# Kernel tuning notes

Measured on AMD Instinct MI355X. Metric: run time of the kernel, lower is better.

Reference implementation:

```python
import jax, jax.numpy as jnp
import numpy as np

L = 2          # lags
D = 16         # latent_size (number of per-channel MLPs)
H = 64         # hidden_dim
SLOPE = 0.2    # LeakyReLU negative slope used by NLayerLeakyMLP


def _forward(x, W0, b0, W1, b1, W2, b2, Wout, bout):
    B, T, _ = x.shape
    nwin = T - L
    # sliding windows of size L+1 along time: [B, nwin, L+1, D]
    idx = jnp.arange(nwin)[:, None] + jnp.arange(L + 1)[None, :]
    w = x[:, idx]
    N = B * nwin
    yy = w[:, :, :L, :].reshape(N, L * D)   # past L steps, flattened
    xx = w[:, :, L, :].reshape(N, D)        # current step, per channel
    # per-channel MLP inputs, stacked over channels: [D, N, L*D+1]
    inputs = jnp.concatenate(
        [jnp.broadcast_to(yy[None], (D, N, L * D)), xx.T[:, :, None]], axis=-1)

    def mlp(inp):  # all D channel-MLPs at once
        h = jax.nn.leaky_relu(jnp.einsum('dni,dhi->dnh', inp, W0) + b0[:, None, :], SLOPE)
        h = jax.nn.leaky_relu(jnp.einsum('dnh,dkh->dnk', h, W1) + b1[:, None, :], SLOPE)
        h = jax.nn.leaky_relu(jnp.einsum('dnh,dkh->dnk', h, W2) + b2[:, None, :], SLOPE)
        return jnp.einsum('dnh,doh->dno', h, Wout) + bout[:, None, :]  # [D, N, 1]

    # d g_i(inputs)/d (last coord) via one forward-mode JVP (replaces the
    # full batched Jacobian + diagonal extraction of the torch version)
    tangent = jnp.zeros_like(inputs).at[..., -1].set(1.0)
    out, dout = jax.jvp(mlp, (inputs,), (tangent,))
    residuals = out[:, :, 0].T.reshape(B, nwin, D)
    logabsdet = jnp.log(jnp.abs(dout[:, :, 0])).sum(0)          # sum over channels -> [N]
    sum_log_abs_det = logabsdet.reshape(B, nwin).sum(1)          # [B]
    return residuals, sum_log_abs_det


def setup_inputs():
    key = jax.random.key(0)
    ks = jax.random.split(key, 9)
    B, T = 32, 512
    in_f = L * D + 1
    s = 0.1
    return {
        "x": jax.random.normal(ks[0], (B, T, D), jnp.float32),
        "W0": jax.random.normal(ks[1], (D, H, in_f), jnp.float32) * s,
        "b0": jax.random.normal(ks[2], (D, H), jnp.float32) * s,
        "W1": jax.random.normal(ks[3], (D, H, H), jnp.float32) * s,
        "b1": jax.random.normal(ks[4], (D, H), jnp.float32) * s,
        "W2": jax.random.normal(ks[5], (D, H, H), jnp.float32) * s,
        "b2": jax.random.normal(ks[6], (D, H), jnp.float32) * s,
        "Wout": jax.random.normal(ks[7], (D, 1, H), jnp.float32) * s,
        "bout": jax.random.normal(ks[8], (D, 1), jnp.float32) * s,
    }


def reference(x, W0, b0, W1, b1, W2, b2, Wout, bout):
    return _forward(x, W0, b0, W1, b1, W2, b2, Wout, bout)
```

## Files before the change

kernel.cpp:

```cpp
#include <hip/hip_runtime.h>
#include <hip/hip_bf16.h>
#include <math.h>

#define NB 32
#define SEQT 512
#define DDIM 16
#define NWIN 510
#define NTOT (NB*NWIN)
#define SLOPE 0.2f
#define NI 3
#define GW 192
#define NGR 85
#define NGP 88

typedef __attribute__((ext_vector_type(8))) short sh8;
typedef __attribute__((ext_vector_type(4))) float f4;

#define W0B_OFF 0
#define W1B_OFF 65536
#define W2B_OFF 196608
#define WCOL_OFF 327680
#define RED_OFF 331776
#define NPREP 164864

static __device__ __forceinline__ unsigned short bfb(float f){
    union { __hip_bfloat16 h; unsigned short u; } cv;
    cv.h = __float2bfloat16(f);
    return cv.u;
}
static __device__ __forceinline__ unsigned pk2(float a, float b){
    return (unsigned)bfb(a) | ((unsigned)bfb(b) << 16);
}

__global__ void prep(const float* __restrict__ W0, const float* __restrict__ W1,
                     const float* __restrict__ W2, unsigned char* __restrict__ wsb){
    int e = blockIdx.x*256 + threadIdx.x;
    if (e < 32768){
        unsigned short* W0b = (unsigned short*)(wsb + W0B_OFF);
        int d = e >> 11, r = e & 2047, h = r >> 5, k = r & 31;
        W0b[e] = bfb(W0[(d*64 + h)*33 + k]);
    } else if (e < 98304){
        ((unsigned short*)(wsb + W1B_OFF))[e - 32768] = bfb(W1[e - 32768]);
    } else if (e < 163840){
        ((unsigned short*)(wsb + W2B_OFF))[e - 98304] = bfb(W2[e - 98304]);
    } else if (e < NPREP){
        int i = e - 163840;
        int d = i >> 6, h = i & 63;
        ((float*)(wsb + WCOL_OFF))[i] = W0[(d*64 + h)*33 + 32];
    }
}

__global__ __launch_bounds__(256, 3) void mlp(
    const float* __restrict__ x,
    const float* __restrict__ bias0, const float* __restrict__ bias1,
    const float* __restrict__ bias2,
    const float* __restrict__ Wout, const float* __restrict__ boutp,
    const unsigned char* __restrict__ wsb,
    float* __restrict__ red, float* __restrict__ out)
{
    __shared__ __align__(16) unsigned char bufA[GW*128];
    __shared__ __align__(16) unsigned char bufB[GW*128];

    const int tid  = threadIdx.x;
    const int lane = tid & 63;
    const int w    = tid >> 6;
    const int nl   = lane & 15;
    const int hi   = lane >> 4;
    const int rsw  = (nl & 7) << 4;

    const int bid = blockIdx.x;
    const int d   = (bid >> 3) & 15;
    const int g   = ((bid >> 7) << 3) | (bid & 7);
    if (g >= NGR) return;

    const unsigned char* W0b = wsb + W0B_OFF + d*4096;
    const unsigned char* W1b = wsb + W1B_OFF + d*8192;
    const unsigned char* W2b = wsb + W2B_OFF + d*8192;

    int   bb[NI], ttv[NI];
    float xxv[NI];
    union { uint4 u; sh8 s; } in[NI];
    #pragma unroll
    for (int i=0;i<NI;++i){
        int n = g*GW + 48*w + nl + 16*i;
        int b = n / NWIN, t = n - b*NWIN;
        bb[i] = b; ttv[i] = t;
        const float* gp = x + (size_t)(b*SEQT + t)*DDIM + 8*hi;
        float4 p0 = ((const float4*)gp)[0];
        float4 p1 = ((const float4*)gp)[1];
        in[i].u.x = pk2(p0.x,p0.y); in[i].u.y = pk2(p0.z,p0.w);
        in[i].u.z = pk2(p1.x,p1.y); in[i].u.w = pk2(p1.z,p1.w);
        xxv[i] = x[(size_t)(b*SEQT + t + 2)*DDIM + d];
    }

    f4 aA[NI][4], aB[NI][4];

    #pragma unroll
    for (int t=0;t<4;++t){
        float4 bv = *(const float4*)(bias0 + d*64 + 16*t + 4*hi);
        #pragma unroll
        for (int i=0;i<NI;++i) aA[i][t] = (f4){bv.x,bv.y,bv.z,bv.w};
    }
    __builtin_amdgcn_s_setprio(1);
    #pragma unroll
    for (int t=0;t<4;++t){
        sh8 af = *(const sh8*)&W0b[((16*t+nl)*32 + 8*hi)*2];
        #pragma unroll
        for (int i=0;i<NI;++i)
            aA[i][t] = __builtin_amdgcn_mfma_f32_16x16x32_bf16(af, in[i].s, aA[i][t], 0,0,0);
    }
    __builtin_amdgcn_s_setprio(0);

    {
        const float* wcolp = (const float*)(wsb + WCOL_OFF) + d*64;
        #pragma unroll
        for (int t=0;t<4;++t){
            float4 wv = *(const float4*)(wcolp + 16*t + 4*hi);
            float wc[4] = {wv.x, wv.y, wv.z, wv.w};
            #pragma unroll
            for (int i=0;i<NI;++i){
                const int row = 48*w + nl + 16*i;
                float v[4], tv[4];
                #pragma unroll
                for (int r=0;r<4;++r){
                    float a = fmaf(wc[r], xxv[i], aA[i][t][r]);
                    v[r]  = fmaxf(a, SLOPE*a);
                    tv[r] = (a >= 0.f) ? wc[r] : SLOPE*wc[r];
                }
                uint2 ph; ph.x = pk2(v[0],v[1]);  ph.y = pk2(v[2],v[3]);
                *(uint2*)&bufA[row*128 + ((32*t + 8*hi) ^ rsw)] = ph;
                uint2 pt; pt.x = pk2(tv[0],tv[1]); pt.y = pk2(tv[2],tv[3]);
                *(uint2*)&bufB[row*128 + ((32*t + 8*hi) ^ rsw)] = pt;
            }
        }
    }

    #pragma unroll
    for (int t=0;t<4;++t){
        float4 bv = *(const float4*)(bias1 + d*64 + 16*t + 4*hi);
        #pragma unroll
        for (int i=0;i<NI;++i){
            aA[i][t] = (f4){bv.x,bv.y,bv.z,bv.w};
            aB[i][t] = (f4){0.f,0.f,0.f,0.f};
        }
    }
    __builtin_amdgcn_s_setprio(1);
    #pragma unroll
    for (int ks=0; ks<2; ++ks){
        sh8 fA[NI], fB[NI];
        #pragma unroll
        for (int i=0;i<NI;++i){
            const int row = 48*w + nl + 16*i;
            fA[i] = *(const sh8*)&bufA[row*128 + ((64*ks + 16*hi) ^ rsw)];
            fB[i] = *(const sh8*)&bufB[row*128 + ((64*ks + 16*hi) ^ rsw)];
        }
        #pragma unroll
        for (int t=0;t<4;++t){
            sh8 af = *(const sh8*)&W1b[((16*t+nl)*64 + 32*ks + 8*hi)*2];
            #pragma unroll
            for (int i=0;i<NI;++i){
                aA[i][t] = __builtin_amdgcn_mfma_f32_16x16x32_bf16(af, fA[i], aA[i][t], 0,0,0);
                aB[i][t] = __builtin_amdgcn_mfma_f32_16x16x32_bf16(af, fB[i], aB[i][t], 0,0,0);
            }
        }
    }
    __builtin_amdgcn_s_setprio(0);
    #pragma unroll
    for (int i=0;i<NI;++i){
        const int row = 48*w + nl + 16*i;
        #pragma unroll
        for (int t=0;t<4;++t){
            float v[4], tv[4];
            #pragma unroll
            for (int r=0;r<4;++r){
                float a = aA[i][t][r];
                v[r] = fmaxf(a, SLOPE*a);
                float q = aB[i][t][r];
                tv[r] = (a >= 0.f) ? q : SLOPE*q;
            }
            uint2 ph; ph.x = pk2(v[0],v[1]); ph.y = pk2(v[2],v[3]);
            *(uint2*)&bufA[row*128 + ((32*t + 8*hi) ^ rsw)] = ph;
            uint2 pt; pt.x = pk2(tv[0],tv[1]); pt.y = pk2(tv[2],tv[3]);
            *(uint2*)&bufB[row*128 + ((32*t + 8*hi) ^ rsw)] = pt;
        }
    }

    #pragma unroll
    for (int t=0;t<4;++t){
        float4 bv = *(const float4*)(bias2 + d*64 + 16*t + 4*hi);
        #pragma unroll
        for (int i=0;i<NI;++i){
            aA[i][t] = (f4){bv.x,bv.y,bv.z,bv.w};
            aB[i][t] = (f4){0.f,0.f,0.f,0.f};
        }
    }
    __builtin_amdgcn_s_setprio(1);
    #pragma unroll
    for (int ks=0; ks<2; ++ks){
        sh8 fA[NI], fB[NI];
        #pragma unroll
        for (int i=0;i<NI;++i){
            const int row = 48*w + nl + 16*i;
            fA[i] = *(const sh8*)&bufA[row*128 + ((64*ks + 16*hi) ^ rsw)];
            fB[i] = *(const sh8*)&bufB[row*128 + ((64*ks + 16*hi) ^ rsw)];
        }
        #pragma unroll
        for (int t=0;t<4;++t){
            sh8 af = *(const sh8*)&W2b[((16*t+nl)*64 + 32*ks + 8*hi)*2];
            #pragma unroll
            for (int i=0;i<NI;++i){
                aA[i][t] = __builtin_amdgcn_mfma_f32_16x16x32_bf16(af, fA[i], aA[i][t], 0,0,0);
                aB[i][t] = __builtin_amdgcn_mfma_f32_16x16x32_bf16(af, fB[i], aB[i][t], 0,0,0);
            }
        }
    }
    __builtin_amdgcn_s_setprio(0);

    float res[NI], dres[NI];
    #pragma unroll
    for (int i=0;i<NI;++i){ res[i] = 0.f; dres[i] = 0.f; }
    #pragma unroll
    for (int t=0;t<4;++t){
        float4 ov = *(const float4*)(Wout + d*64 + 16*t + 4*hi);
        float wo[4] = {ov.x, ov.y, ov.z, ov.w};
        #pragma unroll
        for (int i=0;i<NI;++i){
            #pragma unroll
            for (int r=0;r<4;++r){
                float a  = aA[i][t][r];
                float h3 = fmaxf(a, SLOPE*a);
                res[i] = fmaf(wo[r], h3, res[i]);
                float q  = aB[i][t][r];
                float tv = (a >= 0.f) ? q : SLOPE*q;
                dres[i] = fmaf(wo[r], tv, dres[i]);
            }
        }
    }
    const float bo = boutp[d];
    float la[NI];
    #pragma unroll
    for (int i=0;i<NI;++i){
        res[i]  += __shfl_xor(res[i], 16);  res[i]  += __shfl_xor(res[i], 32);
        dres[i] += __shfl_xor(dres[i], 16); dres[i] += __shfl_xor(dres[i], 32);
        la[i] = __logf(fabsf(dres[i]));
    }
    if (hi == 0){
        #pragma unroll
        for (int i=0;i<NI;++i){
            int n = g*GW + 48*w + nl + 16*i;
            out[(size_t)n*DDIM + d] = res[i] + bo;
        }
    }

    {
        int cb0 = (g*GW) / NWIN;
        float v0 = 0.f, v1 = 0.f;
        #pragma unroll
        for (int i=0;i<NI;++i){
            v0 += (bb[i] == cb0    ) ? la[i] : 0.f;
            v1 += (bb[i] == cb0 + 1) ? la[i] : 0.f;
        }
        #pragma unroll
        for (int s = 1; s < 16; s <<= 1){
            v0 += __shfl_xor(v0, s);
            v1 += __shfl_xor(v1, s);
        }
        if (lane == 0){
            red[((size_t)(g*4 + w)*16 + d)*2 + 0] = v0;
            red[((size_t)(g*4 + w)*16 + d)*2 + 1] = v1;
        }
    }
}

__global__ void final_red(const float* __restrict__ red, float* __restrict__ sld){
    __shared__ float pp[DDIM][16];
    const int b = blockIdx.x;
    const int tid = threadIdx.x;
    const int d = tid & 15, j = tid >> 4;
    float s = 0.f;
    for (int gw = j; gw < NGR*4; gw += 16){
        int g = gw >> 2;
        int cb0 = (g*GW)/NWIN;
        const float* r = red + ((size_t)gw*16 + d)*2;
        if (cb0     == b) s += r[0];
        if (cb0 + 1 == b) s += r[1];
    }
    pp[d][j] = s;
    __syncthreads();
    if (tid < DDIM){
        float a = 0.f;
        #pragma unroll
        for (int k=0;k<16;++k) a += pp[tid][k];
        pp[tid][0] = a;
    }
    __syncthreads();
    if (tid == 0){
        float a = 0.f;
        #pragma unroll
        for (int dd=0; dd<DDIM; ++dd) a += pp[dd][0];
        sld[b] = a;
    }
}

extern "C" void kernel_launch(void* const* d_in, const int* in_sizes, int n_in,
                              void* d_out, int out_size, void* d_ws, size_t ws_size,
                              hipStream_t stream) {
    const float* x    = (const float*)d_in[0];
    const float* W0   = (const float*)d_in[1];
    const float* b0   = (const float*)d_in[2];
    const float* W1   = (const float*)d_in[3];
    const float* b1   = (const float*)d_in[4];
    const float* W2   = (const float*)d_in[5];
    const float* b2   = (const float*)d_in[6];
    const float* Wout = (const float*)d_in[7];
    const float* bout = (const float*)d_in[8];
    float* out = (float*)d_out;
    unsigned char* wsb = (unsigned char*)d_ws;

    prep<<<(NPREP + 255)/256, 256, 0, stream>>>(W0, W1, W2, wsb);

    mlp<<<NGP*DDIM, 256, 0, stream>>>(x, b0, b1, b2, Wout, bout, wsb,
                                      (float*)(wsb + RED_OFF), out);

    final_red<<<NB, 256, 0, stream>>>((const float*)(wsb + RED_OFF),
                                      out + (size_t)NTOT*DDIM);
}
```

Baseline: 42.76 us.

## Fold final reduction into MLP kernel via last-block atomic and widen tiles

Removes the separate final_red launch by having each MLP block increment a global counter, with the last block summing the per-wave partials into the per-batch log-det output. The group width also rises from 192 to 256 rows per block (NI 4), so the grid has no idle padding blocks, with bounds checks on the tail rows. The larger register footprint lowers the launch bound to 2 blocks per CU. The serial tail reduction in one block and the fence/atomic add a little latency.

```diff
diff --git a/kernel.cpp b/kernel.cpp
--- a/kernel.cpp
+++ b/kernel.cpp
@@ -8,10 +8,9 @@
 #define NWIN 510
 #define NTOT (NB*NWIN)
 #define SLOPE 0.2f
-#define NI 3
-#define GW 192
-#define NGR 85
-#define NGP 88
+#define NI 4
+#define GW 256
+#define NGR 64
 
 typedef __attribute__((ext_vector_type(8))) short sh8;
 typedef __attribute__((ext_vector_type(4))) float f4;
@@ -21,6 +20,7 @@
 #define W2B_OFF 196608
 #define WCOL_OFF 327680
 #define RED_OFF 331776
+#define CNT_OFF 364544
 #define NPREP 164864
 
 static __device__ __forceinline__ unsigned short bfb(float f){
@@ -47,19 +47,22 @@
         int i = e - 163840;
         int d = i >> 6, h = i & 63;
         ((float*)(wsb + WCOL_OFF))[i] = W0[(d*64 + h)*33 + 32];
-    }
-}
-
-__global__ __launch_bounds__(256, 3) void mlp(
+    } else if (e == NPREP){
+        *(int*)(wsb + CNT_OFF) = 0;
+    }
+}
+
+__global__ __launch_bounds__(256, 2) void mlp(
     const float* __restrict__ x,
     const float* __restrict__ bias0, const float* __restrict__ bias1,
     const float* __restrict__ bias2,
     const float* __restrict__ Wout, const float* __restrict__ boutp,
-    const unsigned char* __restrict__ wsb,
+    unsigned char* __restrict__ wsb,
     float* __restrict__ red, float* __restrict__ out)
 {
     __shared__ __align__(16) unsigned char bufA[GW*128];
     __shared__ __align__(16) unsigned char bufB[GW*128];
+    __shared__ int lastflag;
 
     const int tid  = threadIdx.x;
     const int lane = tid & 63;
@@ -71,20 +74,22 @@
     const int bid = blockIdx.x;
     const int d   = (bid >> 3) & 15;
     const int g   = ((bid >> 7) << 3) | (bid & 7);
-    if (g >= NGR) return;
 
     const unsigned char* W0b = wsb + W0B_OFF + d*4096;
     const unsigned char* W1b = wsb + W1B_OFF + d*8192;
     const unsigned char* W2b = wsb + W2B_OFF + d*8192;
 
-    int   bb[NI], ttv[NI];
+    int   bb[NI];
+    bool  val[NI];
     float xxv[NI];
     union { uint4 u; sh8 s; } in[NI];
     #pragma unroll
     for (int i=0;i<NI;++i){
-        int n = g*GW + 48*w + nl + 16*i;
-        int b = n / NWIN, t = n - b*NWIN;
-        bb[i] = b; ttv[i] = t;
+        int n = g*GW + 64*w + 16*i + nl;
+        val[i] = (n < NTOT);
+        int ne = val[i] ? n : (NTOT-1);
+        int b = ne / NWIN, t = ne - b*NWIN;
+        bb[i] = b;
         const float* gp = x + (size_t)(b*SEQT + t)*DDIM + 8*hi;
         float4 p0 = ((const float4*)gp)[0];
         float4 p1 = ((const float4*)gp)[1];
@@ -119,7 +124,7 @@
             float wc[4] = {wv.x, wv.y, wv.z, wv.w};
             #pragma unroll
             for (int i=0;i<NI;++i){
-                const int row = 48*w + nl + 16*i;
+                const int row = 64*w + 16*i + nl;
                 float v[4], tv[4];
                 #pragma unroll
                 for (int r=0;r<4;++r){
@@ -150,7 +155,7 @@
         sh8 fA[NI], fB[NI];
         #pragma unroll
         for (int i=0;i<NI;++i){
-            const int row = 48*w + nl + 16*i;
+            const int row = 64*w + 16*i + nl;
             fA[i] = *(const sh8*)&bufA[row*128 + ((64*ks + 16*hi) ^ rsw)];
             fB[i] = *(const sh8*)&bufB[row*128 + ((64*ks + 16*hi) ^ rsw)];
         }
@@ -167,7 +172,7 @@
     __builtin_amdgcn_s_setprio(0);
     #pragma unroll
     for (int i=0;i<NI;++i){
-        const int row = 48*w + nl + 16*i;
+        const int row = 64*w + 16*i + nl;
         #pragma unroll
         for (int t=0;t<4;++t){
             float v[4], tv[4];
@@ -200,7 +205,7 @@
         sh8 fA[NI], fB[NI];
         #pragma unroll
         for (int i=0;i<NI;++i){
-            const int row = 48*w + nl + 16*i;
+            const int row = 64*w + 16*i + nl;
             fA[i] = *(const sh8*)&bufA[row*128 + ((64*ks + 16*hi) ^ rsw)];
             fB[i] = *(const sh8*)&bufB[row*128 + ((64*ks + 16*hi) ^ rsw)];
         }
@@ -247,8 +252,10 @@
     if (hi == 0){
         #pragma unroll
         for (int i=0;i<NI;++i){
-            int n = g*GW + 48*w + nl + 16*i;
-            out[(size_t)n*DDIM + d] = res[i] + bo;
+            if (val[i]){
+                int n = g*GW + 64*w + 16*i + nl;
+                out[(size_t)n*DDIM + d] = res[i] + bo;
+            }
         }
     }
 
@@ -257,8 +264,10 @@
         float v0 = 0.f, v1 = 0.f;
         #pragma unroll
         for (int i=0;i<NI;++i){
-            v0 += (bb[i] == cb0    ) ? la[i] : 0.f;
-            v1 += (bb[i] == cb0 + 1) ? la[i] : 0.f;
+            if (val[i]){
+                v0 += (bb[i] == cb0    ) ? la[i] : 0.f;
+                v1 += (bb[i] == cb0 + 1) ? la[i] : 0.f;
+            }
         }
         #pragma unroll
         for (int s = 1; s < 16; s <<= 1){
@@ -270,35 +279,46 @@
             red[((size_t)(g*4 + w)*16 + d)*2 + 1] = v1;
         }
     }
-}
-
-__global__ void final_red(const float* __restrict__ red, float* __restrict__ sld){
-    __shared__ float pp[DDIM][16];
-    const int b = blockIdx.x;
-    const int tid = threadIdx.x;
-    const int d = tid & 15, j = tid >> 4;
-    float s = 0.f;
-    for (int gw = j; gw < NGR*4; gw += 16){
-        int g = gw >> 2;
-        int cb0 = (g*GW)/NWIN;
-        const float* r = red + ((size_t)gw*16 + d)*2;
-        if (cb0     == b) s += r[0];
-        if (cb0 + 1 == b) s += r[1];
-    }
-    pp[d][j] = s;
-    __syncthreads();
-    if (tid < DDIM){
-        float a = 0.f;
-        #pragma unroll
-        for (int k=0;k<16;++k) a += pp[tid][k];
-        pp[tid][0] = a;
-    }
+
     __syncthreads();
     if (tid == 0){
-        float a = 0.f;
-        #pragma unroll
-        for (int dd=0; dd<DDIM; ++dd) a += pp[dd][0];
-        sld[b] = a;
+        __threadfence();
+        int old = atomicAdd((int*)(wsb + CNT_OFF), 1);
+        lastflag = (old == NGR*DDIM - 1);
+        if (lastflag) *(int*)(wsb + CNT_OFF) = 0;
+    }
+    __syncthreads();
+    if (lastflag){
+        __threadfence();
+        float* sg = (float*)bufA;
+        {
+            int gw = tid;
+            float s0 = 0.f, s1 = 0.f;
+            #pragma unroll
+            for (int dd=0; dd<DDIM; ++dd){
+                s0 += red[((size_t)gw*16 + dd)*2 + 0];
+                s1 += red[((size_t)gw*16 + dd)*2 + 1];
+            }
+            sg[gw] = s0; sg[256 + gw] = s1;
+        }
+        __syncthreads();
+        if (tid < NB){
+            const int b = tid;
+            float s = 0.f;
+            #pragma unroll
+            for (int gg=0; gg<NGR; ++gg){
+                int cb0 = (gg*GW)/NWIN;
+                if (cb0 == b){
+                    #pragma unroll
+                    for (int ww=0; ww<4; ++ww) s += sg[gg*4 + ww];
+                }
+                if (cb0 + 1 == b){
+                    #pragma unroll
+                    for (int ww=0; ww<4; ++ww) s += sg[256 + gg*4 + ww];
+                }
+            }
+            out[(size_t)NTOT*DDIM + b] = s;
+        }
     }
 }
 
@@ -317,11 +337,8 @@
     float* out = (float*)d_out;
     unsigned char* wsb = (unsigned char*)d_ws;
 
-    prep<<<(NPREP + 255)/256, 256, 0, stream>>>(W0, W1, W2, wsb);
-
-    mlp<<<NGP*DDIM, 256, 0, stream>>>(x, b0, b1, b2, Wout, bout, wsb,
+    prep<<<(NPREP + 256)/256, 256, 0, stream>>>(W0, W1, W2, wsb);
+
+    mlp<<<NGR*DDIM, 256, 0, stream>>>(x, b0, b1, b2, Wout, bout, wsb,
                                       (float*)(wsb + RED_OFF), out);
-
-    final_red<<<NB, 256, 0, stream>>>((const float*)(wsb + RED_OFF),
-                                      out + (size_t)NTOT*DDIM);
-}
+}
```

After: 69.73 us. 1.63x slower.
